# Performance work log

Measured on AMD Instinct MI355X. Metric: run time of the kernel, lower is better.

## Reference

```python
import math
import jax, jax.numpy as jnp
import numpy as np

NBINS = 10
MAX_ANGLE = math.pi
KERNEL = 8
POOL_PAD = 1
POOL_STRIDE = 1


def setup_inputs() -> dict:
    key = jax.random.key(0)
    x = jax.random.normal(key, (32, 1, 512, 512), dtype=jnp.float32)
    # Sobel buffer: mat stacked with its transpose -> [2, 1, 3, 3]
    mat = jnp.array([[1.0, 0.0, -1.0], [2.0, 0.0, -2.0], [1.0, 0.0, -1.0]], dtype=jnp.float32)
    weight = jnp.stack([mat, mat.T])[:, None, :, :]
    return {"x": x, "weight": weight}


def reference(x, weight):
    # Sobel gradients: conv2d, stride 1, padding 1 (cross-correlation, same as torch)
    gxy = jax.lax.conv_general_dilated(
        x, weight, window_strides=(1, 1),
        padding=[(1, 1), (1, 1)],
        dimension_numbers=("NCHW", "OIHW", "NCHW"))  # [N,2,H,W]

    norm = jnp.sqrt(gxy[:, 0] ** 2 + gxy[:, 1] ** 2)[:, None]        # [N,1,H,W]
    phase = jnp.arctan2(gxy[:, 0], gxy[:, 1])                        # [N,H,W]
    phase_int = (phase / MAX_ANGLE * NBINS)[:, None]                 # [N,1,H,W]

    # torch `%` is remainder (sign of divisor) == jnp.mod
    b = jnp.floor(phase_int) % NBINS
    t = jnp.ceil(phase_int) % NBINS
    f = phase_int % NBINS
    t_v = norm * (1.0 - (t - f))
    b_v = norm * (1.0 - (f - b))

    idx_b = jnp.floor(phase_int).astype(jnp.int32) % NBINS           # [N,1,H,W]
    idx_t = jnp.ceil(phase_int).astype(jnp.int32) % NBINS

    # scatter into nbins channels: out starts at zero, scatter_ (set) then
    # scatter_add_ -> equivalent to sum of the two one-hot contributions
    bins = jnp.arange(NBINS, dtype=jnp.int32)[None, :, None, None]   # [1,nbins,1,1]
    out = jnp.where(bins == idx_b, b_v, 0.0) + jnp.where(bins == idx_t, t_v, 0.0)  # [N,nbins,H,W]

    # AvgPool2d(kernel=8, stride=1, padding=1, count_include_pad=True)
    summed = jax.lax.reduce_window(
        out, 0.0, jax.lax.add,
        window_dimensions=(1, 1, KERNEL, KERNEL),
        window_strides=(1, 1, POOL_STRIDE, POOL_STRIDE),
        padding=[(0, 0), (0, 0), (POOL_PAD, POOL_PAD), (POOL_PAD, POOL_PAD)])
    return summed / float(KERNEL * KERNEL)
```

## Files before the change

### kernel.cpp

```cpp
#include <hip/hip_runtime.h>
#include <math.h>

#define NB 10
#define H 512
#define W 512
#define HW (H * W)
#define OH 507
#define OW 507
#define TW 32
#define TH 16
#define HC 39
#define HR 23
#define IC 41
#define IR 25
#define BD 512
#define HSTRIDE (HR * HC)
#define HISTF (NB * HSTRIDE + 2)
#define GX 16
#define GY 32
#define NIMG 32
#define NWG (GX * GY * NIMG)

__device__ __forceinline__ float f32mod10(float a) {
    float r = fmodf(a, 10.0f);
    if (r < 0.0f) r = __fadd_rn(r, 10.0f);
    return r;
}

struct alignas(4) f4u { float a, b, c, d; };

__global__ __launch_bounds__(BD, 8)
void hog_fused(const float* __restrict__ x, float* __restrict__ out) {
    __shared__ __align__(16) float hist[HISTF];
    __shared__ __align__(16) float xin[IR * IC];

    const int orig = blockIdx.x;
    const int swz  = (orig & 7) * (NWG / 8) + (orig >> 3);
    const int tx   = swz & (GX - 1);
    const int ty   = (swz >> 4) & (GY - 1);
    const int n    = swz >> 9;

    const int tid = threadIdx.x;
    const int ox0 = tx * TW;
    const int oy0 = ty * TH;
    const float* __restrict__ xp = x + (size_t)n * HW;

    const int i1 = tid, i2 = tid + BD;
    int r1 = i1 / IC, c1 = i1 - r1 * IC;
    int r2 = i2 / IC, c2 = i2 - r2 * IC;
    int gy1 = oy0 - 2 + r1, gx1 = ox0 - 2 + c1;
    int gy2 = oy0 - 2 + r2, gx2 = ox0 - 2 + c2;
    const bool v1 = (unsigned)gy1 < H && (unsigned)gx1 < W;
    const bool v2 = (unsigned)gy2 < H && (unsigned)gx2 < W;
    float pv1 = v1 ? xp[gy1 * W + gx1] : 0.0f;
    float pv2 = v2 ? xp[gy2 * W + gx2] : 0.0f;
    float pv3 = 0.0f;
    if (tid == 0 && (unsigned)(oy0 + 22) < H && (unsigned)(ox0 + 38) < W)
        pv3 = xp[(oy0 + 22) * W + (ox0 + 38)];

    {
        float4* h4 = (float4*)hist;
        for (int i = tid; i < HISTF / 4; i += BD)
            h4[i] = make_float4(0.f, 0.f, 0.f, 0.f);
    }
    xin[i1] = pv1;
    xin[i2] = pv2;
    if (tid == 0) xin[1024] = pv3;
    __syncthreads();

    if (tid < 12 * HC) {
        const int rp = tid / HC;
        const int hc = tid - rp * HC;
        const int hr0 = rp * 2;
        const float* xb = &xin[hr0 * IC + hc];

        auto pixel = [&](int hr, float a00, float a01, float a02,
                                 float a10, float a12,
                                 float a20, float a21, float a22) {
            const int hy = oy0 - 1 + hr, hx = ox0 - 1 + hc;
            if ((unsigned)hy >= H || (unsigned)hx >= W) return;
            float gxv = __fadd_rn(a00, -a02);
            gxv = __fadd_rn(gxv, __fmul_rn(2.0f, a10));
            gxv = __fadd_rn(gxv, -__fmul_rn(2.0f, a12));
            gxv = __fadd_rn(gxv, a20);
            gxv = __fadd_rn(gxv, -a22);
            float gyv = __fadd_rn(a00, __fmul_rn(2.0f, a01));
            gyv = __fadd_rn(gyv, a02);
            gyv = __fadd_rn(gyv, -a20);
            gyv = __fadd_rn(gyv, -__fmul_rn(2.0f, a21));
            gyv = __fadd_rn(gyv, -a22);

            float ay_ = fabsf(gxv), ax_ = fabsf(gyv);
            float hi = fmaxf(ax_, ay_), lo = fminf(ax_, ay_);
            if (hi == 0.0f) return;
            float nrm = __builtin_amdgcn_sqrtf(
                __fadd_rn(__fmul_rn(gxv, gxv), __fmul_rn(gyv, gyv)));

            bool exact = (hi < 1e-30f) || (hi > 1e30f);
            float pint = 0.0f;
            if (!exact) {
                float t  = lo * __builtin_amdgcn_rcpf(hi);
                bool red = t > 0.41421356f;
                float u  = red ? (t - 1.0f) * __builtin_amdgcn_rcpf(t + 1.0f) : t;
                float z  = u * u;
                float pl = ((8.05374449538e-2f * z - 1.38776856032e-1f) * z
                            + 1.99777106478e-1f) * z - 3.33329491539e-1f;
                float a  = fmaf(u * z, pl, u);
                if (red) a += 0.78539816339744831f;
                if (ay_ > ax_) a = 1.57079632679489662f - a;
                if (gyv < 0.0f) a = 3.14159265358979324f - a;
                float ph = (gxv < 0.0f) ? -a : a;
                pint = ph * 3.18309886183790672f;
                if (fabsf(pint - rintf(pint)) < 1e-4f) exact = true;
            }

            float b_v, t_v;
            int ib, it;
            if (exact) {
                float phf = (float)atan2((double)gxv, (double)gyv);
                float pe  = __fmul_rn(__fdiv_rn(phf, (float)3.14159265358979323846), 10.0f);
                float bfv = floorf(pe), tfv = ceilf(pe);
                float fm = f32mod10(pe), bm = f32mod10(bfv), tm = f32mod10(tfv);
                t_v = __fmul_rn(nrm, __fsub_rn(1.0f, __fsub_rn(tm, fm)));
                b_v = __fmul_rn(nrm, __fsub_rn(1.0f, __fsub_rn(fm, bm)));
                ib = (((int)bfv % NB) + NB) % NB;
                it = (((int)tfv % NB) + NB) % NB;
            } else {
                float bfv  = floorf(pint);
                float frac = pint - bfv;
                float fm   = (pint < 0.0f) ? pint + 10.0f : pint;
                b_v = nrm * (1.0f - frac);
                int bi = (int)bfv;
                ib = (bi < 0) ? bi + 10 : bi;
                if (ib == 9) { it = 0;      t_v = nrm * (1.0f + fm); }
                else         { it = ib + 1; t_v = nrm * frac; }
            }
            const int cell = hr * HC + hc;
            if (ib == it) {
                hist[ib * HSTRIDE + cell] = __fadd_rn(b_v, t_v);
            } else {
                hist[ib * HSTRIDE + cell] = b_v;
                hist[it * HSTRIDE + cell] = t_v;
            }
        };

        float x00 = xb[0],      x01 = xb[1],          x02 = xb[2];
        float x10 = xb[IC],     x11 = xb[IC + 1],     x12 = xb[IC + 2];
        float x20 = xb[2 * IC], x21 = xb[2 * IC + 1], x22 = xb[2 * IC + 2];
        pixel(hr0, x00, x01, x02, x10, x12, x20, x21, x22);
        if (hr0 + 1 < HR) {
            float x30 = xb[3 * IC], x31 = xb[3 * IC + 1], x32 = xb[3 * IC + 2];
            pixel(hr0 + 1, x10, x11, x12, x20, x22, x30, x31, x32);
        }
    }
    __syncthreads();

    for (int q = tid; q < NB * HC; q += BD) {
        int b = q / HC, hc = q - (q / HC) * HC;
        float* col = &hist[b * HSTRIDE + hc];
        float s = 0.0f;
        #pragma unroll
        for (int hr = 0; hr < 8; ++hr) s += col[hr * HC];
        float s0 = s;
        #pragma unroll 4
        for (int i = 1; i < TH; ++i) {
            s += col[(i + 7) * HC] - col[(i - 1) * HC];
            col[(i - 1) * HC] = s;
        }
        col[22 * HC] = s0;
    }
    __syncthreads();

    float* __restrict__ outn = out + (size_t)n * (NB * OH * OW);
    for (int u = tid; u < NB * TH * 8; u += BD) {
        int b = u >> 7, i = (u >> 3) & 15, q = u & 7;
        const float* cs = &hist[b * HSTRIDE
                                + (i == 0 ? 22 * HC : (i - 1) * HC) + 4 * q];
        float p0 = cs[0], p1 = cs[1], p2 = cs[2],  p3 = cs[3];
        float p4 = cs[4], p5 = cs[5], p6 = cs[6],  p7 = cs[7];
        float p8 = cs[8], p9 = cs[9], p10 = cs[10];
        float o0 = ((p0 + p1) + (p2 + p3)) + ((p4 + p5) + (p6 + p7));
        float o1 = o0 - p0 + p8;
        float o2 = o1 - p1 + p9;
        float o3 = o2 - p2 + p10;
        int oy = oy0 + i;
        if (oy < OH) {
            int oxg = ox0 + 4 * q;
            float* po = outn + (size_t)(b * OH + oy) * OW + oxg;
            const float s = 1.0f / 64.0f;
            if (oxg + 3 < OW) {
                *reinterpret_cast<f4u*>(po) = f4u{o0 * s, o1 * s, o2 * s, o3 * s};
            } else {
                float ov[4] = {o0, o1, o2, o3};
                #pragma unroll
                for (int j = 0; j < 4; ++j)
                    if (oxg + j < OW) po[j] = ov[j] * s;
            }
        }
    }
}

extern "C" void kernel_launch(void* const* d_in, const int* in_sizes, int n_in,
                              void* d_out, int out_size, void* d_ws, size_t ws_size,
                              hipStream_t stream) {
    const float* x = (const float*)d_in[0];
    float* out = (float*)d_out;
    hog_fused<<<dim3(NWG), dim3(BD), 0, stream>>>(x, out);
}
```

Before: 129.9 us.

## Pad histogram rows to 40 floats and vectorize vertical and horizontal pooling passes

Pads the shared-memory histogram row stride from 39 to 40 floats so rows are 16-byte aligned. The vertical box-sum pass now has 400 threads each handle a float4 column group over 4 output rows, instead of 390 threads each walking a scalar column serially. The horizontal pass reads three float4 values instead of eleven scalars. This cuts LDS instruction count and shortens the serial sliding-window dependency chain. It recomputes the 8-row initial sums per group, which adds some redundant adds, and it may change bank-conflict patterns.

```diff
diff --git a/kernel.cpp b/kernel.cpp
--- a/kernel.cpp
+++ b/kernel.cpp
@@ -10,12 +10,13 @@
 #define TW 32
 #define TH 16
 #define HC 39
+#define HCP 40
 #define HR 23
 #define IC 41
 #define IR 25
 #define BD 512
-#define HSTRIDE (HR * HC)
-#define HISTF (NB * HSTRIDE + 2)
+#define BSTRIDE (HR * HCP)
+#define HISTF (NB * BSTRIDE)
 #define GX 16
 #define GY 32
 #define NIMG 32
@@ -135,12 +136,12 @@
                 if (ib == 9) { it = 0;      t_v = nrm * (1.0f + fm); }
                 else         { it = ib + 1; t_v = nrm * frac; }
             }
-            const int cell = hr * HC + hc;
+            const int cell = hr * HCP + hc;
             if (ib == it) {
-                hist[ib * HSTRIDE + cell] = __fadd_rn(b_v, t_v);
+                hist[ib * BSTRIDE + cell] = __fadd_rn(b_v, t_v);
             } else {
-                hist[ib * HSTRIDE + cell] = b_v;
-                hist[it * HSTRIDE + cell] = t_v;
+                hist[ib * BSTRIDE + cell] = b_v;
+                hist[it * BSTRIDE + cell] = t_v;
             }
         };
 
@@ -155,34 +156,42 @@
     }
     __syncthreads();
 
-    for (int q = tid; q < NB * HC; q += BD) {
-        int b = q / HC, hc = q - (q / HC) * HC;
-        float* col = &hist[b * HSTRIDE + hc];
-        float s = 0.0f;
+    if (tid < NB * 10 * 4) {
+        const int g  = tid & 3;
+        const int q  = tid >> 2;
+        const int c4 = q % 10, b = q / 10;
+        float4* col = (float4*)&hist[b * BSTRIDE + c4 * 4];
+        const int i0 = 4 * g;
+        float4 v[11];
         #pragma unroll
-        for (int hr = 0; hr < 8; ++hr) s += col[hr * HC];
-        float s0 = s;
-        #pragma unroll 4
-        for (int i = 1; i < TH; ++i) {
-            s += col[(i + 7) * HC] - col[(i - 1) * HC];
-            col[(i - 1) * HC] = s;
-        }
-        col[22 * HC] = s0;
+        for (int r = 0; r < 11; ++r) v[r] = col[(i0 + r) * 10];
+        float4 s = v[0];
+        #pragma unroll
+        for (int r = 1; r < 8; ++r) {
+            s.x += v[r].x; s.y += v[r].y; s.z += v[r].z; s.w += v[r].w;
+        }
+        col[(i0 == 0 ? 22 : i0 - 1) * 10] = s;
+        #pragma unroll
+        for (int k = 1; k < 4; ++k) {
+            s.x += v[k + 7].x - v[k - 1].x;
+            s.y += v[k + 7].y - v[k - 1].y;
+            s.z += v[k + 7].z - v[k - 1].z;
+            s.w += v[k + 7].w - v[k - 1].w;
+            col[(i0 + k - 1) * 10] = s;
+        }
     }
     __syncthreads();
 
     float* __restrict__ outn = out + (size_t)n * (NB * OH * OW);
     for (int u = tid; u < NB * TH * 8; u += BD) {
         int b = u >> 7, i = (u >> 3) & 15, q = u & 7;
-        const float* cs = &hist[b * HSTRIDE
-                                + (i == 0 ? 22 * HC : (i - 1) * HC) + 4 * q];
-        float p0 = cs[0], p1 = cs[1], p2 = cs[2],  p3 = cs[3];
-        float p4 = cs[4], p5 = cs[5], p6 = cs[6],  p7 = cs[7];
-        float p8 = cs[8], p9 = cs[9], p10 = cs[10];
-        float o0 = ((p0 + p1) + (p2 + p3)) + ((p4 + p5) + (p6 + p7));
-        float o1 = o0 - p0 + p8;
-        float o2 = o1 - p1 + p9;
-        float o3 = o2 - p2 + p10;
+        const float4* cs4 = (const float4*)&hist[b * BSTRIDE
+                                + (i == 0 ? 22 : i - 1) * HCP + 4 * q];
+        float4 A = cs4[0], B = cs4[1], C = cs4[2];
+        float o0 = ((A.x + A.y) + (A.z + A.w)) + ((B.x + B.y) + (B.z + B.w));
+        float o1 = o0 - A.x + C.x;
+        float o2 = o1 - A.y + C.y;
+        float o3 = o2 - A.z + C.z;
         int oy = oy0 + i;
         if (oy < OH) {
             int oxg = ox0 + 4 * q;
```

Result: no change. 132.4 us (+1.9%).
